# Kernel tuning notes

Measured on AMD Instinct MI355X. Metric: run time of the kernel, lower is better.

## Reference

```python
import jax, jax.numpy as jnp
import numpy as np

B = 524288
HIDDEN = 128
EXP_MAX = 88.0

def setup_inputs() -> dict:
    key = jax.random.key(0)
    ks = jax.random.split(key, 5)
    t = jax.random.uniform(ks[0], (B,), dtype=jnp.float32)
    u = jax.random.uniform(ks[1], (B, 10), dtype=jnp.float32)
    p = jax.random.uniform(ks[2], (37,), dtype=jnp.float32)
    W1 = jax.random.normal(ks[3], (5, HIDDEN), dtype=jnp.float32) * 0.1
    b1 = jnp.zeros((HIDDEN,), jnp.float32)
    W2 = jax.random.normal(ks[4], (HIDDEN, 2), dtype=jnp.float32) * 0.1
    b2 = jnp.zeros((2,), jnp.float32)
    return {"t": t, "u": u, "p": p, "W1": W1, "b1": b1, "W2": W2, "b2": b2}

def reference(t, u, p, W1, b1, W2, b2):
    # state unpack: u[:, i] are per-instance scalars, shape [B]
    Qmt, Qav, Qtc, Qpv, Vlv, Vao, Vvc, Vrv, Vpa, Vpu = (u[:, i] for i in range(10))
    (Elvf, Eao, Evc, Ervf, Epa, Epu, Rmt, Rav, Rsys, Rtc, Rpv, Rpul,
     Lmt, Lav, Ltc, Lpv, Vdlvf, Vdao, Vdvc, Vdrvf, Vdpa, Vdpu,
     P0lvf, P0rvf, lamlvf, lamrvf, Espt, V0lvf, V0rvf, P0spt, P0pcd,
     V0spt, V0pcd, lamspt, lampcd, Vdspt, Pth) = (p[i] for i in range(37))

    # cardiac driver function
    e = jnp.exp(-80.0 * (jnp.mod(t, 0.75) - 0.375) ** 2)

    # small surrogate MLP: [B,5] -> [B,2] (tanh hidden)
    inp = jnp.stack([Vlv, Vao, Vvc, Vrv, Vpa], axis=-1)
    h = jnp.tanh(inp @ W1 + b1)
    z = h @ W2 + b2
    Pperi, Vspt = z[:, 0], z[:, 1]

    Vlvf = Vlv - Vspt
    Vrvf = Vrv + Vspt
    exp_lv = jnp.exp(jnp.minimum(lamlvf * (Vlvf - V0lvf), EXP_MAX))
    exp_rv = jnp.exp(jnp.minimum(lamrvf * (Vrvf - V0rvf), EXP_MAX))

    Plvf = e * Elvf * (Vlvf - Vdlvf) + (1.0 - e) * P0lvf * (exp_lv - 1.0)
    Prvf = e * Ervf * (Vrvf - Vdrvf) + (1.0 - e) * P0rvf * (exp_rv - 1.0)
    Plv = Plvf + Pperi
    Prv = Prvf + Pperi
    Pao = Eao * (Vao - Vdao)
    Pvc = Evc * (Vvc - Vdvc)
    Ppa = Epa * (Vpa - Vdpa) + Pth
    Ppu = Epu * (Vpu - Vdpu) + Pth
    Qsys = (Pao - Pvc) / Rsys
    Qpul = (Ppa - Ppu) / Rpul

    # valve flows with open/closed branching (computed with un-clamped Q)
    du0 = jnp.where((Ppu - Plv > 0) | (Qmt > 0), (Ppu - Plv - Qmt * Rmt) / Lmt, 0.0)
    du1 = jnp.where((Plv - Pao > 0) | (Qav > 0), (Plv - Pao - Qav * Rav) / Lav, 0.0)
    du2 = jnp.where((Pvc - Prv > 0) | (Qtc > 0), (Pvc - Prv - Qtc * Rtc) / Ltc, 0.0)
    du3 = jnp.where((Prv - Ppa > 0) | (Qpv > 0), (Prv - Ppa - Qpv * Rpv) / Lpv, 0.0)

    # volumes use clamped (non-negative) flows
    Qmt_c = jnp.maximum(Qmt, 0.0)
    Qav_c = jnp.maximum(Qav, 0.0)
    Qtc_c = jnp.maximum(Qtc, 0.0)
    Qpv_c = jnp.maximum(Qpv, 0.0)
    du4 = Qmt_c - Qav_c
    du5 = Qav_c - Qsys
    du6 = Qsys - Qtc_c
    du7 = Qtc_c - Qpv_c
    du8 = Qpv_c - Qpul
    du9 = Qpul - Qmt_c

    return jnp.stack([du0, du1, du2, du3, du4, du5, du6, du7, du8, du9], axis=-1)
```

## Files before the change

### kernel.cpp

```cpp
#include <hip/hip_runtime.h>

#define B_TOTAL 524288
#define HID 128
#define ROWS 4
#define BLK 256
#define NBLK (B_TOTAL / ROWS / BLK)

static __device__ __forceinline__ float fast_exp2(float x) {
    float r;
    asm("v_exp_f32 %0, %1" : "=v"(r) : "v"(x));
    return r;
}

__global__ void pack_w(const float* __restrict__ W1, const float* __restrict__ b1,
                       const float* __restrict__ W2, float* __restrict__ wp) {
    const int j = threadIdx.x;
    if (j < HID) {
        const float s = 2.8853900817779268f;
        wp[j * 8 + 0] = W1[0 * HID + j] * s;
        wp[j * 8 + 1] = W1[1 * HID + j] * s;
        wp[j * 8 + 2] = W1[2 * HID + j] * s;
        wp[j * 8 + 3] = W1[3 * HID + j] * s;
        wp[j * 8 + 4] = W1[4 * HID + j] * s;
        wp[j * 8 + 5] = b1[j] * s;
        wp[j * 8 + 6] = W2[j * 2 + 0];
        wp[j * 8 + 7] = W2[j * 2 + 1];
    }
}

__global__ __launch_bounds__(BLK, 2) void ode_kernel(
    const float* __restrict__ t,
    const float* __restrict__ u,
    const float* __restrict__ p,
    const float* __restrict__ wp,
    const float* __restrict__ b2,
    float* __restrict__ out)
{
    const int g = blockIdx.x * BLK + threadIdx.x;

    float ub[ROWS * 10];
    const float4* u4 = reinterpret_cast<const float4*>(u + (size_t)g * (ROWS * 10));
#pragma unroll
    for (int i = 0; i < 10; ++i) reinterpret_cast<float4*>(ub)[i] = u4[i];

    const float4 tv4 = *reinterpret_cast<const float4*>(t + (size_t)g * ROWS);
    const float tv[ROWS] = {tv4.x, tv4.y, tv4.z, tv4.w};

    const float b20 = b2[0], b21 = b2[1];
    float z0[ROWS], z1[ROWS];
#pragma unroll
    for (int r = 0; r < ROWS; ++r) { z0[r] = b20; z1[r] = b21; }

    const float4* wp4 = reinterpret_cast<const float4*>(wp);
#pragma unroll 4
    for (int j = 0; j < HID; ++j) {
        const float4 wa = wp4[2 * j];
        const float4 wb = wp4[2 * j + 1];
#pragma unroll
        for (int r = 0; r < ROWS; ++r) {
            float y = wb.y;
            y = fmaf(ub[r * 10 + 4], wa.x, y);
            y = fmaf(ub[r * 10 + 5], wa.y, y);
            y = fmaf(ub[r * 10 + 6], wa.z, y);
            y = fmaf(ub[r * 10 + 7], wa.w, y);
            y = fmaf(ub[r * 10 + 8], wb.x, y);
            const float e2 = fast_exp2(y);
            const float th = 1.0f - 2.0f * __builtin_amdgcn_rcpf(e2 + 1.0f);
            z0[r] = fmaf(th, wb.z, z0[r]);
            z1[r] = fmaf(th, wb.w, z1[r]);
        }
    }

    const float Elvf = p[0],  Eao = p[1],   Evc = p[2],   Ervf = p[3];
    const float Epa  = p[4],  Epu = p[5];
    const float Rmt  = p[6],  Rav = p[7],   Rsys = p[8],  Rtc = p[9];
    const float Rpv  = p[10], Rpul = p[11];
    const float Lmt  = p[12], Lav = p[13],  Ltc = p[14],  Lpv = p[15];
    const float Vdlvf = p[16], Vdao = p[17], Vdvc = p[18], Vdrvf = p[19];
    const float Vdpa  = p[20], Vdpu = p[21];
    const float P0lvf = p[22], P0rvf = p[23];
    const float lamlvf = p[24], lamrvf = p[25];
    const float V0lvf = p[27], V0rvf = p[28];
    const float Pth   = p[36];

    const float L2E = 1.4426950408889634f;
    const float inv_Rsys = __builtin_amdgcn_rcpf(Rsys);
    const float inv_Rpul = __builtin_amdgcn_rcpf(Rpul);
    const float inv_Lmt  = __builtin_amdgcn_rcpf(Lmt);
    const float inv_Lav  = __builtin_amdgcn_rcpf(Lav);
    const float inv_Ltc  = __builtin_amdgcn_rcpf(Ltc);
    const float inv_Lpv  = __builtin_amdgcn_rcpf(Lpv);
    const float laml_l2e = lamlvf * L2E;
    const float lamr_l2e = lamrvf * L2E;
    const float CLAMP2 = 88.0f * L2E;

    float du[ROWS * 10];
#pragma unroll
    for (int r = 0; r < ROWS; ++r) {
        const float Qmt = ub[r * 10 + 0], Qav = ub[r * 10 + 1];
        const float Qtc = ub[r * 10 + 2], Qpv = ub[r * 10 + 3];
        const float Vlv = ub[r * 10 + 4], Vao = ub[r * 10 + 5];
        const float Vvc = ub[r * 10 + 6], Vrv = ub[r * 10 + 7];
        const float Vpa = ub[r * 10 + 8], Vpu = ub[r * 10 + 9];
        const float Pperi = z0[r], Vspt = z1[r];

        const float m  = (tv[r] >= 0.75f) ? (tv[r] - 0.75f) : tv[r];
        const float dd = m - 0.375f;
        const float e  = fast_exp2(dd * dd * (-80.0f * L2E));

        const float Vlvf = Vlv - Vspt;
        const float Vrvf = Vrv + Vspt;
        const float exp_lv = fast_exp2(fminf(laml_l2e * (Vlvf - V0lvf), CLAMP2));
        const float exp_rv = fast_exp2(fminf(lamr_l2e * (Vrvf - V0rvf), CLAMP2));
        const float ome = 1.0f - e;
        const float Plvf = e * Elvf * (Vlvf - Vdlvf) + ome * P0lvf * (exp_lv - 1.0f);
        const float Prvf = e * Ervf * (Vrvf - Vdrvf) + ome * P0rvf * (exp_rv - 1.0f);
        const float Plv = Plvf + Pperi;
        const float Prv = Prvf + Pperi;
        const float Pao = Eao * (Vao - Vdao);
        const float Pvc = Evc * (Vvc - Vdvc);
        const float Ppa = fmaf(Epa, Vpa - Vdpa, Pth);
        const float Ppu = fmaf(Epu, Vpu - Vdpu, Pth);
        const float Qsys = (Pao - Pvc) * inv_Rsys;
        const float Qpul = (Ppa - Ppu) * inv_Rpul;

        du[r * 10 + 0] = ((Ppu - Plv > 0.0f) || (Qmt > 0.0f)) ? (Ppu - Plv - Qmt * Rmt) * inv_Lmt : 0.0f;
        du[r * 10 + 1] = ((Plv - Pao > 0.0f) || (Qav > 0.0f)) ? (Plv - Pao - Qav * Rav) * inv_Lav : 0.0f;
        du[r * 10 + 2] = ((Pvc - Prv > 0.0f) || (Qtc > 0.0f)) ? (Pvc - Prv - Qtc * Rtc) * inv_Ltc : 0.0f;
        du[r * 10 + 3] = ((Prv - Ppa > 0.0f) || (Qpv > 0.0f)) ? (Prv - Ppa - Qpv * Rpv) * inv_Lpv : 0.0f;

        const float Qmt_c = fmaxf(Qmt, 0.0f);
        const float Qav_c = fmaxf(Qav, 0.0f);
        const float Qtc_c = fmaxf(Qtc, 0.0f);
        const float Qpv_c = fmaxf(Qpv, 0.0f);
        du[r * 10 + 4] = Qmt_c - Qav_c;
        du[r * 10 + 5] = Qav_c - Qsys;
        du[r * 10 + 6] = Qsys - Qtc_c;
        du[r * 10 + 7] = Qtc_c - Qpv_c;
        du[r * 10 + 8] = Qpv_c - Qpul;
        du[r * 10 + 9] = Qpul - Qmt_c;
    }

    float4* o4 = reinterpret_cast<float4*>(out + (size_t)g * (ROWS * 10));
#pragma unroll
    for (int i = 0; i < 10; ++i) o4[i] = reinterpret_cast<const float4*>(du)[i];
}

extern "C" void kernel_launch(void* const* d_in, const int* in_sizes, int n_in,
                              void* d_out, int out_size, void* d_ws, size_t ws_size,
                              hipStream_t stream) {
    const float* t  = (const float*)d_in[0];
    const float* u  = (const float*)d_in[1];
    const float* p  = (const float*)d_in[2];
    const float* W1 = (const float*)d_in[3];
    const float* b1 = (const float*)d_in[4];
    const float* W2 = (const float*)d_in[5];
    const float* b2 = (const float*)d_in[6];
    float* out = (float*)d_out;
    float* wp  = (float*)d_ws;

    pack_w<<<1, HID, 0, stream>>>(W1, b1, W2, wp);
    ode_kernel<<<NBLK, BLK, 0, stream>>>(t, u, p, wp, b2, out);
}
```

Baseline: 111.0 us.

## Use packed float2 FMAs for MLP and drop weight-packing kernel

```diff
diff --git a/kernel.cpp b/kernel.cpp
--- a/kernel.cpp
+++ b/kernel.cpp
@@ -6,33 +6,32 @@
 #define BLK 256
 #define NBLK (B_TOTAL / ROWS / BLK)
 
+typedef float v2f __attribute__((ext_vector_type(2)));
+
 static __device__ __forceinline__ float fast_exp2(float x) {
     float r;
     asm("v_exp_f32 %0, %1" : "=v"(r) : "v"(x));
     return r;
 }
+static __device__ __forceinline__ v2f splat2(float x) { v2f r; r.x = x; r.y = x; return r; }
 
-__global__ void pack_w(const float* __restrict__ W1, const float* __restrict__ b1,
-                       const float* __restrict__ W2, float* __restrict__ wp) {
-    const int j = threadIdx.x;
-    if (j < HID) {
-        const float s = 2.8853900817779268f;
-        wp[j * 8 + 0] = W1[0 * HID + j] * s;
-        wp[j * 8 + 1] = W1[1 * HID + j] * s;
-        wp[j * 8 + 2] = W1[2 * HID + j] * s;
-        wp[j * 8 + 3] = W1[3 * HID + j] * s;
-        wp[j * 8 + 4] = W1[4 * HID + j] * s;
-        wp[j * 8 + 5] = b1[j] * s;
-        wp[j * 8 + 6] = W2[j * 2 + 0];
-        wp[j * 8 + 7] = W2[j * 2 + 1];
-    }
+#if __has_builtin(__builtin_elementwise_fma)
+static __device__ __forceinline__ v2f fma2(v2f a, v2f b, v2f c) {
+    return __builtin_elementwise_fma(a, b, c);
 }
+#else
+static __device__ __forceinline__ v2f fma2(v2f a, v2f b, v2f c) {
+    v2f r; r.x = fmaf(a.x, b.x, c.x); r.y = fmaf(a.y, b.y, c.y); return r;
+}
+#endif
 
 __global__ __launch_bounds__(BLK, 2) void ode_kernel(
     const float* __restrict__ t,
     const float* __restrict__ u,
     const float* __restrict__ p,
-    const float* __restrict__ wp,
+    const float* __restrict__ W1,
+    const float* __restrict__ b1,
+    const float* __restrict__ W2,
     const float* __restrict__ b2,
     float* __restrict__ out)
 {
@@ -46,30 +45,60 @@
     const float4 tv4 = *reinterpret_cast<const float4*>(t + (size_t)g * ROWS);
     const float tv[ROWS] = {tv4.x, tv4.y, tv4.z, tv4.w};
 
-    const float b20 = b2[0], b21 = b2[1];
-    float z0[ROWS], z1[ROWS];
+    v2f vin[2][5];
 #pragma unroll
-    for (int r = 0; r < ROWS; ++r) { z0[r] = b20; z1[r] = b21; }
+    for (int pr = 0; pr < 2; ++pr)
+#pragma unroll
+        for (int k = 0; k < 5; ++k) {
+            v2f v; v.x = ub[(2 * pr) * 10 + 4 + k]; v.y = ub[(2 * pr + 1) * 10 + 4 + k];
+            vin[pr][k] = v;
+        }
 
-    const float4* wp4 = reinterpret_cast<const float4*>(wp);
-#pragma unroll 4
-    for (int j = 0; j < HID; ++j) {
-        const float4 wa = wp4[2 * j];
-        const float4 wb = wp4[2 * j + 1];
+    const float S2L2E = 2.8853900817779268f;
+    const v2f s2v = splat2(S2L2E);
+
+    v2f z0p[2], z1p[2];
+    z0p[0] = z0p[1] = splat2(b2[0]);
+    z1p[0] = z1p[1] = splat2(b2[1]);
+
+#pragma unroll 2
+    for (int jg = 0; jg < HID; jg += 4) {
+        float w1c[4][5];
 #pragma unroll
-        for (int r = 0; r < ROWS; ++r) {
-            float y = wb.y;
-            y = fmaf(ub[r * 10 + 4], wa.x, y);
-            y = fmaf(ub[r * 10 + 5], wa.y, y);
-            y = fmaf(ub[r * 10 + 6], wa.z, y);
-            y = fmaf(ub[r * 10 + 7], wa.w, y);
-            y = fmaf(ub[r * 10 + 8], wb.x, y);
-            const float e2 = fast_exp2(y);
-            const float th = 1.0f - 2.0f * __builtin_amdgcn_rcpf(e2 + 1.0f);
-            z0[r] = fmaf(th, wb.z, z0[r]);
-            z1[r] = fmaf(th, wb.w, z1[r]);
+        for (int k = 0; k < 5; ++k) {
+            const float4 w4 = *reinterpret_cast<const float4*>(W1 + k * HID + jg);
+            w1c[0][k] = w4.x; w1c[1][k] = w4.y; w1c[2][k] = w4.z; w1c[3][k] = w4.w;
+        }
+        const float4 b14 = *reinterpret_cast<const float4*>(b1 + jg);
+        const float bb[4] = {b14.x, b14.y, b14.z, b14.w};
+        const float4 w2a = *reinterpret_cast<const float4*>(W2 + 2 * jg);
+        const float4 w2b = *reinterpret_cast<const float4*>(W2 + 2 * jg + 4);
+        const float w20[4] = {w2a.x, w2a.z, w2b.x, w2b.z};
+        const float w21[4] = {w2a.y, w2a.w, w2b.y, w2b.w};
+
+#pragma unroll
+        for (int jj = 0; jj < 4; ++jj) {
+#pragma unroll
+            for (int pr = 0; pr < 2; ++pr) {
+                v2f y = splat2(bb[jj]);
+                y = fma2(vin[pr][0], splat2(w1c[jj][0]), y);
+                y = fma2(vin[pr][1], splat2(w1c[jj][1]), y);
+                y = fma2(vin[pr][2], splat2(w1c[jj][2]), y);
+                y = fma2(vin[pr][3], splat2(w1c[jj][3]), y);
+                y = fma2(vin[pr][4], splat2(w1c[jj][4]), y);
+                y = y * s2v;
+                v2f e2; e2.x = fast_exp2(y.x); e2.y = fast_exp2(y.y);
+                e2 = e2 + splat2(1.0f);
+                v2f rc; rc.x = __builtin_amdgcn_rcpf(e2.x); rc.y = __builtin_amdgcn_rcpf(e2.y);
+                const v2f th = fma2(rc, splat2(-2.0f), splat2(1.0f));
+                z0p[pr] = fma2(th, splat2(w20[jj]), z0p[pr]);
+                z1p[pr] = fma2(th, splat2(w21[jj]), z1p[pr]);
+            }
         }
     }
+
+    const float z0[ROWS] = {z0p[0].x, z0p[0].y, z0p[1].x, z0p[1].y};
+    const float z1[ROWS] = {z1p[0].x, z1p[0].y, z1p[1].x, z1p[1].y};
 
     const float Elvf = p[0],  Eao = p[1],   Evc = p[2],   Ervf = p[3];
     const float Epa  = p[4],  Epu = p[5];
@@ -157,8 +186,6 @@
     const float* W2 = (const float*)d_in[5];
     const float* b2 = (const float*)d_in[6];
     float* out = (float*)d_out;
-    float* wp  = (float*)d_ws;
 
-    pack_w<<<1, HID, 0, stream>>>(W1, b1, W2, wp);
-    ode_kernel<<<NBLK, BLK, 0, stream>>>(t, u, p, wp, b2, out);
+    ode_kernel<<<NBLK, BLK, 0, stream>>>(t, u, p, W1, b1, W2, b2, out);
 }
```

Result: faster. 106.9 us (-3.8%).
